# Kernel tuning notes

Measured on AMD Instinct MI355X. Metric: run time of the kernel, lower is better.

## Reference

```python
import jax, jax.numpy as jnp
import numpy as np

N_ITEMS = 2000
N_STORAGE = 4094
N_LOCS = N_STORAGE + 2  # storage locations + start + end
E = 4_194_304
HID = 32


def setup_inputs() -> dict:
    rng = np.random.default_rng(0)
    etype = rng.integers(0, 3, size=E)  # 0: loc-loc, 1: item-item, 2: item-loc
    src = np.empty(E, dtype=np.int64)
    dst = np.empty(E, dtype=np.int64)
    m0, m1, m2 = (etype == 0), (etype == 1), (etype == 2)
    src[m0] = rng.integers(N_ITEMS, N_ITEMS + N_LOCS, m0.sum())
    dst[m0] = rng.integers(N_ITEMS, N_ITEMS + N_LOCS, m0.sum())
    src[m1] = rng.integers(0, N_ITEMS, m1.sum())
    dst[m1] = rng.integers(0, N_ITEMS, m1.sum())
    src[m2] = rng.integers(0, N_ITEMS, m2.sum())
    dst[m2] = rng.integers(N_ITEMS, N_ITEMS + N_STORAGE, m2.sum())
    edge_index = jnp.asarray(np.stack([src, dst]))
    edge_attr = jnp.asarray(rng.random((E, 2)).astype(np.float32))
    edge_type_mask = jnp.asarray(np.eye(3, dtype=bool)[etype])
    k1, k2 = jax.random.split(jax.random.key(0))
    W1 = jax.random.normal(k1, (3, HID), jnp.float32) * 0.5
    b1 = jnp.zeros((HID,), jnp.float32)
    W2 = jax.random.normal(k2, (HID, 1), jnp.float32) * 0.5
    b2 = jnp.zeros((1,), jnp.float32)
    return {
        "edge_index": edge_index,
        "edge_attr": edge_attr,
        "edge_type_mask": edge_type_mask,
        "n_items": N_ITEMS,
        "n_storage": N_STORAGE,
        "n_locs": N_LOCS,
        "W1": W1, "b1": b1, "W2": W2, "b2": b2,
    }


def reference(edge_index, edge_attr, edge_type_mask, n_items, n_storage, n_locs,
              W1, b1, W2, b2):
    src, dst = edge_index[0], edge_index[1]

    # --- loc-loc distance matrix: scatter masked edges into [n_locs, n_locs] ---
    ls, ld = src - n_items, dst - n_items
    v = edge_type_mask[:, 0] & (ls >= 0) & (ls < n_locs) & (ld >= 0) & (ld < n_locs)
    ls = jnp.where(v, ls, n_locs)  # invalid -> out of bounds, dropped by scatter
    ld = jnp.where(v, ld, n_locs)
    loc_mat = jnp.zeros((n_locs, n_locs), edge_attr.dtype).at[ls, ld].set(
        edge_attr[:, 0], mode="drop")

    # --- item-item sequence-count matrix: [n_items, n_items] ---
    v = edge_type_mask[:, 1] & (src >= 0) & (src < n_items) & (dst >= 0) & (dst < n_items)
    is_ = jnp.where(v, src, n_items)
    id_ = jnp.where(v, dst, n_items)
    seq_mat = jnp.zeros((n_items, n_items), edge_attr.dtype).at[is_, id_].set(
        edge_attr[:, 1], mode="drop")

    # --- item -> storage-location assignment: [n_items] int ---
    li = dst - n_items
    v = edge_type_mask[:, 2] & (src >= 0) & (src < n_items) & (li >= 0) & (li < n_storage)
    ii = jnp.where(v, src, n_items)
    item_to_loc = jnp.zeros((n_items,), jnp.int32).at[ii].set(
        jnp.where(v, li, 0).astype(jnp.int32), mode="drop")

    # --- item_item_dist = sum_{i,j: seq>0} seq_mat[i,j] * loc_mat[loc_i, loc_j] ---
    gathered = loc_mat[item_to_loc][:, item_to_loc]  # [n_items, n_items]
    item_item_dist = jnp.sum(jnp.where(seq_mat > 0, seq_mat * gathered, 0.0))

    # --- start / end depot distances (start_idx = n_storage, end_idx = n_storage+1) ---
    start_dist = jnp.sum(loc_mat[n_storage, item_to_loc]) if n_storage < n_locs else jnp.float32(0.0)
    end_dist = jnp.sum(loc_mat[item_to_loc, n_storage + 1]) if n_storage + 1 < n_locs else jnp.float32(0.0)

    comps = jnp.stack([item_item_dist, start_dist, end_dist])[None, :]  # [1, 3]
    h = jax.nn.relu(comps @ W1 + b1)
    pred = h @ W2 + b2  # [1, 1]
    return pred.squeeze()
```

## Files before the change

kernel.cpp:

```cpp
#include <hip/hip_runtime.h>

#define N_ITEMS   2000
#define N_STORAGE 4094
#define N_LOCS    4096
#define E_EDGES   4194304
#define LOCD      2048
#define NBLKB     512
#define BCAP      8192
#define SGRP      500
#define LGRP      512
#define NG        1012
#define SCAP      3456
#define LCAP      3456

typedef unsigned long long u64;
typedef unsigned int u32;
typedef int   vi4 __attribute__((ext_vector_type(4)));
typedef float vf4 __attribute__((ext_vector_type(4)));

__device__ __forceinline__ int wave_incl_scan(int v) {
    #pragma unroll
    for (int o = 1; o < 64; o <<= 1) {
        int u = __shfl_up(v, o);
        if ((threadIdx.x & 63) >= o) v += u;
    }
    return v;
}


__global__ __launch_bounds__(1024)
void bin_all(const int* __restrict__ src, const int* __restrict__ dst,
             const float* __restrict__ attr, u64* __restrict__ seqrec,
             u32* __restrict__ locrec, int* __restrict__ pfxS, int* __restrict__ pfxL,
             int* __restrict__ slab, int* __restrict__ flags4) {
    __shared__ int lwin[N_ITEMS];
    __shared__ int cnt[NG];
    __shared__ int exclS[SGRP];
    __shared__ int exclL[LGRP];
    __shared__ int wsum[16];
    __shared__ int totSL[2];
    __shared__ u64 sseq[SCAP];
    __shared__ u32 sloc[LCAP];
    int t = threadIdx.x;
    for (int i = t; i < N_ITEMS; i += 1024) lwin[i] = -1;
    for (int i = t; i < NG; i += 1024) cnt[i] = 0;
    if (t < 32) flags4[blockIdx.x * 32 + t] = 0;
    int rel0 = t * 8;
    int base = blockIdx.x * BCAP + rel0;
    vi4 sa = __builtin_nontemporal_load((const vi4*)&src[base]);
    vi4 sb = __builtin_nontemporal_load((const vi4*)&src[base + 4]);
    vi4 da = __builtin_nontemporal_load((const vi4*)&dst[base]);
    vi4 db = __builtin_nontemporal_load((const vi4*)&dst[base + 4]);
    vf4 a0 = __builtin_nontemporal_load((const vf4*)&attr[base * 2]);
    vf4 a1 = __builtin_nontemporal_load((const vf4*)&attr[base * 2 + 4]);
    vf4 a2 = __builtin_nontemporal_load((const vf4*)&attr[base * 2 + 8]);
    vf4 a3 = __builtin_nontemporal_load((const vf4*)&attr[base * 2 + 12]);
    __syncthreads();
    int ss[8] = {sa[0], sa[1], sa[2], sa[3], sb[0], sb[1], sb[2], sb[3]};
    int dd[8] = {da[0], da[1], da[2], da[3], db[0], db[1], db[2], db[3]};
    float v1[8] = {a0[1], a0[3], a1[1], a1[3], a2[1], a2[3], a3[1], a3[3]};
    u32 meta[8], aux[8], val[8];
    #pragma unroll
    for (int k = 0; k < 8; ++k) {
        int s = ss[k], d = dd[k];
        u32 m = 0xFFFFFFFFu, ic = 0, vv = 0;
        if ((unsigned)s < N_ITEMS) {
            if ((unsigned)d < N_ITEMS) {
                int g = s >> 2;
                m = ((u32)atomicAdd(&cnt[g], 1) << 10) | (u32)g;
                ic = ((u32)(s & 3) << 24) | ((u32)d << 13) | (u32)(rel0 + k);
                vv = __float_as_uint(v1[k]);
            } else {
                unsigned li = (unsigned)(d - N_ITEMS);
                if (li < N_STORAGE) atomicMax(&lwin[s], base + k);
            }
        } else {
            unsigned ls = (unsigned)(s - N_ITEMS), ld = (unsigned)(d - N_ITEMS);
            if (ls < N_LOCS && ld < N_LOCS) {
                int g = SGRP + (int)(ls >> 3);
                m = ((u32)atomicAdd(&cnt[g], 1) << 10) | (u32)g;
                ic = ((ls & 7u) << 25) | (ld << 13) | (u32)(rel0 + k);
            }
        }
        meta[k] = m;
        aux[k] = ic;
        val[k] = vv;
    }
    __syncthreads();
    int v;
    if (t < 512) v = (t < SGRP) ? cnt[t] : 0;
    else         v = cnt[t - 12];
    int inc = wave_incl_scan(v);
    if ((t & 63) == 63) wsum[t >> 6] = inc;
    __syncthreads();
    int w = t >> 6, lo = (t < 512) ? 0 : 8, woff = 0;
    #pragma unroll
    for (int k = 0; k < 16; ++k) woff += (k >= lo && k < w) ? wsum[k] : 0;
    int ex = inc - v + woff;
    if (t < SGRP) {
        exclS[t] = ex;
        pfxS[t * NBLKB + blockIdx.x] = ex;
    } else if (t >= 512) {
        exclL[t - 512] = ex;
        pfxL[(t - 512) * NBLKB + blockIdx.x] = ex;
    }
    if (t == 0) {
        int t0 = 0, t1 = 0;
        #pragma unroll
        for (int k = 0; k < 8; ++k) { t0 += wsum[k]; t1 += wsum[k + 8]; }
        pfxS[SGRP * NBLKB + blockIdx.x] = t0;
        pfxL[LGRP * NBLKB + blockIdx.x] = t1;
        totSL[0] = t0;
        totSL[1] = t1;
    }
    __syncthreads();
    u64* srb = seqrec + (size_t)blockIdx.x * BCAP;
    u32* lrb = locrec + (size_t)blockIdx.x * BCAP;
    #pragma unroll
    for (int k = 0; k < 8; ++k) {
        u32 m = meta[k];
        if (m != 0xFFFFFFFFu) {
            int g = (int)(m & 1023u), rank = (int)(m >> 10);
            if (g < SGRP) {
                int idx = exclS[g] + rank;
                u64 rec = ((u64)aux[k] << 32) | (u64)val[k];
                if (idx < SCAP) sseq[idx] = rec;
                else            srb[idx] = rec;
            } else {
                int idx = exclL[g - SGRP] + rank;
                if (idx < LCAP) sloc[idx] = aux[k];
                else            lrb[idx] = aux[k];
            }
        }
    }
    __syncthreads();
    int totS = min(totSL[0], SCAP), totL = min(totSL[1], LCAP);
    for (int i = t; i < totS; i += 1024) srb[i] = sseq[i];
    for (int i = t; i < totL; i += 1024) lrb[i] = sloc[i];
    for (int i = t; i < N_ITEMS; i += 1024) slab[blockIdx.x * 2048 + i] = lwin[i];
}

__global__ __launch_bounds__(1024)
void item_reduce(const int* __restrict__ slab, const int* __restrict__ dst,
                 int* __restrict__ item_loc, int* __restrict__ used_row,
                 int* __restrict__ used_col) {
    __shared__ int red[16][64];
    int t = threadIdx.x;
    int lane = t & 63, sub = t >> 6;
    int i = blockIdx.x * 64 + lane;
    int m = -1;
    for (int b = sub; b < NBLKB; b += 16)
        m = max(m, slab[b * 2048 + i]);
    red[sub][lane] = m;
    __syncthreads();
    if (sub == 0 && i < N_ITEMS) {
        #pragma unroll
        for (int k = 1; k < 16; ++k) m = max(m, red[k][lane]);
        int loc = (m >= 0) ? (dst[m] - N_ITEMS) : 0;
        item_loc[i] = loc;
        used_row[loc] = 1;
        used_col[loc] = 1;
    }
    if (blockIdx.x == 0 && t == 0) {
        used_row[N_STORAGE] = 1;
        used_col[N_STORAGE + 1] = 1;
    }
}

__global__ __launch_bounds__(1024)
void remap_fused(const int* __restrict__ used_row, const int* __restrict__ used_col,
                 const int* __restrict__ item_loc, int* __restrict__ rrow,
                 int* __restrict__ rcol, int* __restrict__ item_rr,
                 int* __restrict__ item_rc, int* __restrict__ rse) {
    __shared__ int wsA[16], wsB[16];
    int t = threadIdx.x;
    vi4 ur = *(const vi4*)&used_row[t * 4];
    vi4 uc = *(const vi4*)&used_col[t * 4];
    int sA = ur[0] + ur[1] + ur[2] + ur[3];
    int sB = uc[0] + uc[1] + uc[2] + uc[3];
    int iA = wave_incl_scan(sA);
    int iB = wave_incl_scan(sB);
    if ((t & 63) == 63) { wsA[t >> 6] = iA; wsB[t >> 6] = iB; }
    __syncthreads();
    int w = t >> 6, oA = 0, oB = 0;
    #pragma unroll
    for (int k = 0; k < 16; ++k) {
        oA += (k < w) ? wsA[k] : 0;
        oB += (k < w) ? wsB[k] : 0;
    }
    int runA = iA - sA + oA;
    int runB = iB - sB + oB;
    vi4 rr4, rc4;
    #pragma unroll
    for (int j = 0; j < 4; ++j) {
        runA += ur[j]; rr4[j] = ur[j] ? runA : 0;
        runB += uc[j]; rc4[j] = uc[j] ? runB : 0;
    }
    *(vi4*)&rrow[t * 4] = rr4;
    *(vi4*)&rcol[t * 4] = rc4;
    __syncthreads();
    for (int i = t; i < N_ITEMS; i += 1024) {
        int loc = item_loc[i];
        item_rr[i] = rrow[loc] - 1;
        item_rc[i] = rcol[loc] - 1;
    }
    if (t == 0) {
        rse[0] = rrow[N_STORAGE] - 1;
        rse[1] = rcol[N_STORAGE + 1] - 1;
    }
}

__global__ __launch_bounds__(1024)
void loc_dedup(const u32* __restrict__ locrec, const int* __restrict__ pfxL,
               const float* __restrict__ attr, const int* __restrict__ rrow,
               const int* __restrict__ rcol, float* __restrict__ locf) {
    __shared__ u32 win[8 * 2048];
    __shared__ short rcol_s[N_LOCS];
    __shared__ int rrow8[8];
    int t = threadIdx.x, g = blockIdx.x;
    if (t < 8) rrow8[t] = rrow[g * 8 + t];
    for (int i = t; i < 8 * 2048; i += 1024) win[i] = 0;
    for (int i = t; i < N_LOCS; i += 1024) rcol_s[i] = (short)rcol[i];
    __syncthreads();
    int b = t >> 1, q = t & 1;
    int s0 = pfxL[g * NBLKB + b], s1 = pfxL[(g + 1) * NBLKB + b];
    const u32* rb = locrec + (size_t)b * BCAP;
    u32 kb = ((u32)b << 13) + 1;
    for (int r = s0 + q; r < s1; r += 2) {
        u32 rec = rb[r];
        int il = (int)(rec >> 25);
        if (rrow8[il] <= 0) continue;
        int rc = rcol_s[(rec >> 13) & 4095u];
        if (rc <= 0) continue;
        atomicMax(&win[il * 2048 + rc - 1], kb + (rec & 8191u));
    }
    __syncthreads();
    for (int il = 0; il < 8; ++il) {
        int cr = rrow8[il];
        if (cr <= 0) continue;
        const u32* wrow = &win[il * 2048];
        float* orow = locf + (size_t)(cr - 1) * LOCD;
        for (int i = t; i < 2048; i += 1024) {
            u32 w = wrow[i];
            orow[i] = w ? attr[2 * (int)(w - 1)] : 0.f;
        }
    }
}

__global__ __launch_bounds__(1024)
void seq_dedup(const u64* __restrict__ seqrec, const int* __restrict__ pfxS,
               const float* __restrict__ locf, const int* __restrict__ item_rr,
               const int* __restrict__ item_rc, const int* __restrict__ rse,
               float* __restrict__ gpart) {
    __shared__ u64 win[4 * 2048];
    __shared__ short rcs[N_ITEMS];
    __shared__ int rrs[4];
    __shared__ float red[16][3];
    int t = threadIdx.x, g = blockIdx.x;
    for (int i = t; i < 4 * 2048; i += 1024) win[i] = 0;
    for (int i = t; i < N_ITEMS; i += 1024) rcs[i] = (short)item_rc[i];
    if (t < 4) rrs[t] = item_rr[g * 4 + t];
    __syncthreads();
    int b = t >> 1, q = t & 1;
    int s0 = pfxS[g * NBLKB + b], s1 = pfxS[(g + 1) * NBLKB + b];
    const u64* rb = seqrec + (size_t)b * BCAP;
    u64 kb = ((u64)((u32)b << 13) + 1) << 32;
    for (int r = s0 + q; r < s1; r += 2) {
        u64 rec = rb[r];
        u32 ax = (u32)(rec >> 32);
        int slot = (((int)(ax >> 24) & 3) << 11) | (int)((ax >> 13) & 2047u);
        atomicMax(&win[slot], kb + ((u64)(ax & 8191u) << 32) + (rec & 0xFFFFFFFFull));
    }
    __syncthreads();
    float acc = 0.f, sd = 0.f, ed = 0.f;
    for (int i = t; i < 4 * 2048; i += 1024) {
        u64 w = win[i];
        if (w) {
            float seq = __uint_as_float((u32)(w & 0xFFFFFFFFull));
            if (seq > 0.f)
                acc += seq * locf[(size_t)rrs[i >> 11] * LOCD + (int)rcs[i & 2047]];
        }
    }
    if (t < 4) {
        sd = locf[(size_t)rse[0] * LOCD + (int)rcs[g * 4 + t]];
        ed = locf[(size_t)rrs[t] * LOCD + rse[1]];
    }
    #pragma unroll
    for (int o = 32; o > 0; o >>= 1) {
        acc += __shfl_down(acc, o);
        sd  += __shfl_down(sd, o);
        ed  += __shfl_down(ed, o);
    }
    if ((t & 63) == 0) { red[t >> 6][0] = acc; red[t >> 6][1] = sd; red[t >> 6][2] = ed; }
    __syncthreads();
    if (t == 0) {
        float a = 0.f, bb = 0.f, c = 0.f;
        #pragma unroll
        for (int k = 0; k < 16; ++k) { a += red[k][0]; bb += red[k][1]; c += red[k][2]; }
        gpart[g * 3 + 0] = a;
        gpart[g * 3 + 1] = bb;
        gpart[g * 3 + 2] = c;
    }
}

__global__ void final_mlp(const float* __restrict__ gpart, const float* __restrict__ W1,
                          const float* __restrict__ b1, const float* __restrict__ W2,
                          const float* __restrict__ b2, float* __restrict__ out) {
    __shared__ float s0[4], s1[4], s2[4];
    int t = threadIdx.x;
    float a = 0.f, b = 0.f, c = 0.f;
    for (int i = t; i < SGRP; i += 256) {
        a += gpart[i * 3 + 0];
        b += gpart[i * 3 + 1];
        c += gpart[i * 3 + 2];
    }
    #pragma unroll
    for (int o = 32; o > 0; o >>= 1) {
        a += __shfl_down(a, o);
        b += __shfl_down(b, o);
        c += __shfl_down(c, o);
    }
    if ((t & 63) == 0) { s0[t >> 6] = a; s1[t >> 6] = b; s2[t >> 6] = c; }
    __syncthreads();
    float v = 0.f;
    if (t < 32) {
        float ca = s0[0] + s0[1] + s0[2] + s0[3];
        float cb = s1[0] + s1[1] + s1[2] + s1[3];
        float cc = s2[0] + s2[1] + s2[2] + s2[3];
        float h = ca * W1[t] + cb * W1[32 + t] + cc * W1[64 + t] + b1[t];
        h = fmaxf(h, 0.f);
        v = h * W2[t];
    }
    #pragma unroll
    for (int o = 32; o > 0; o >>= 1) v += __shfl_down(v, o);
    if (t == 0) out[0] = v + b2[0];
}

extern "C" void kernel_launch(void* const* d_in, const int* in_sizes, int n_in,
                              void* d_out, int out_size, void* d_ws, size_t ws_size,
                              hipStream_t stream) {
    const int*   eidx = (const int*)d_in[0];
    const int*   src  = eidx;
    const int*   dst  = eidx + E_EDGES;
    const float* attr = (const float*)d_in[1];
    const float* W1 = (const float*)d_in[6];
    const float* b1 = (const float*)d_in[7];
    const float* W2 = (const float*)d_in[8];
    const float* b2 = (const float*)d_in[9];

    u64*   seqrec   = (u64*)d_ws;
    u32*   locrec   = (u32*)(seqrec + (size_t)NBLKB * BCAP);
    float* locf     = (float*)(locrec + (size_t)NBLKB * BCAP);
    int*   used_row = (int*)(locf + (size_t)LOCD * LOCD);
    int*   used_col = used_row + N_LOCS;
    int*   rrow     = used_col + N_LOCS;
    int*   rcol     = rrow + N_LOCS;
    int*   pfxS     = rcol + N_LOCS;
    int*   pfxL     = pfxS + (SGRP + 1) * NBLKB;
    int*   slab     = pfxL + (LGRP + 1) * NBLKB;
    int*   item_loc = slab + NBLKB * 2048;
    int*   item_rr  = item_loc + N_ITEMS;
    int*   item_rc  = item_rr + N_ITEMS;
    int*   rse      = item_rc + N_ITEMS;
    float* gpart    = (float*)(rse + 2);

    bin_all    <<<NBLKB, 1024, 0, stream>>>(src, dst, attr, seqrec, locrec,
                                            pfxS, pfxL, slab, used_row);
    item_reduce<<<32, 1024, 0, stream>>>(slab, dst, item_loc, used_row, used_col);
    remap_fused<<<1, 1024, 0, stream>>>(used_row, used_col, item_loc, rrow, rcol,
                                        item_rr, item_rc, rse);
    loc_dedup  <<<LGRP, 1024, 0, stream>>>(locrec, pfxL, attr, rrow, rcol, locf);
    seq_dedup  <<<SGRP, 1024, 0, stream>>>(seqrec, pfxS, locf,
                                           item_rr, item_rc, rse, gpart);
    final_mlp  <<<1, 256, 0, stream>>>(gpart, W1, b1, W2, b2, (float*)d_out);
}
```

Measured before the change: 79.83 us.

## Fuse remap prefix scans into loc_dedup and seq_dedup kernels

Removes the single-block remap_fused kernel and has every block of loc_dedup and seq_dedup recompute the used_row/used_col prefix scans in shared memory. Item row/column remaps are derived locally from item_loc. This eliminates one kernel launch and a serialized one-block stage, along with its global intermediate arrays. The cost is redundant scan work and extra barriers in every block.

```diff
diff --git a/kernel.cpp b/kernel.cpp
--- a/kernel.cpp
+++ b/kernel.cpp
@@ -44,7 +44,7 @@
     int t = threadIdx.x;
     for (int i = t; i < N_ITEMS; i += 1024) lwin[i] = -1;
     for (int i = t; i < NG; i += 1024) cnt[i] = 0;
-    if (t < 32) flags4[blockIdx.x * 32 + t] = 0;
+    if (t < 16) flags4[blockIdx.x * 16 + t] = 0;
     int rel0 = t * 8;
     int base = blockIdx.x * BCAP + rel0;
     vi4 sa = __builtin_nontemporal_load((const vi4*)&src[base]);
@@ -168,59 +168,46 @@
 }
 
 __global__ __launch_bounds__(1024)
-void remap_fused(const int* __restrict__ used_row, const int* __restrict__ used_col,
-                 const int* __restrict__ item_loc, int* __restrict__ rrow,
-                 int* __restrict__ rcol, int* __restrict__ item_rr,
-                 int* __restrict__ item_rc, int* __restrict__ rse) {
-    __shared__ int wsA[16], wsB[16];
-    int t = threadIdx.x;
-    vi4 ur = *(const vi4*)&used_row[t * 4];
-    vi4 uc = *(const vi4*)&used_col[t * 4];
-    int sA = ur[0] + ur[1] + ur[2] + ur[3];
-    int sB = uc[0] + uc[1] + uc[2] + uc[3];
-    int iA = wave_incl_scan(sA);
-    int iB = wave_incl_scan(sB);
-    if ((t & 63) == 63) { wsA[t >> 6] = iA; wsB[t >> 6] = iB; }
-    __syncthreads();
-    int w = t >> 6, oA = 0, oB = 0;
-    #pragma unroll
-    for (int k = 0; k < 16; ++k) {
-        oA += (k < w) ? wsA[k] : 0;
-        oB += (k < w) ? wsB[k] : 0;
-    }
-    int runA = iA - sA + oA;
-    int runB = iB - sB + oB;
-    vi4 rr4, rc4;
-    #pragma unroll
-    for (int j = 0; j < 4; ++j) {
-        runA += ur[j]; rr4[j] = ur[j] ? runA : 0;
-        runB += uc[j]; rc4[j] = uc[j] ? runB : 0;
-    }
-    *(vi4*)&rrow[t * 4] = rr4;
-    *(vi4*)&rcol[t * 4] = rc4;
-    __syncthreads();
-    for (int i = t; i < N_ITEMS; i += 1024) {
-        int loc = item_loc[i];
-        item_rr[i] = rrow[loc] - 1;
-        item_rc[i] = rcol[loc] - 1;
-    }
-    if (t == 0) {
-        rse[0] = rrow[N_STORAGE] - 1;
-        rse[1] = rcol[N_STORAGE + 1] - 1;
-    }
-}
-
-__global__ __launch_bounds__(1024)
 void loc_dedup(const u32* __restrict__ locrec, const int* __restrict__ pfxL,
-               const float* __restrict__ attr, const int* __restrict__ rrow,
-               const int* __restrict__ rcol, float* __restrict__ locf) {
+               const float* __restrict__ attr, const int* __restrict__ used_row,
+               const int* __restrict__ used_col, float* __restrict__ locf) {
     __shared__ u32 win[8 * 2048];
     __shared__ short rcol_s[N_LOCS];
     __shared__ int rrow8[8];
+    __shared__ int ws[16];
     int t = threadIdx.x, g = blockIdx.x;
-    if (t < 8) rrow8[t] = rrow[g * 8 + t];
+    vi4 uc = *(const vi4*)&used_col[t * 4];
+    int sB = uc[0] + uc[1] + uc[2] + uc[3];
+    int iB = wave_incl_scan(sB);
+    if ((t & 63) == 63) ws[t >> 6] = iB;
+    __syncthreads();
+    int w = t >> 6, oB = 0;
+    #pragma unroll
+    for (int k = 0; k < 16; ++k) oB += (k < w) ? ws[k] : 0;
+    int runB = iB - sB + oB;
+    #pragma unroll
+    for (int j = 0; j < 4; ++j) {
+        runB += uc[j];
+        rcol_s[t * 4 + j] = uc[j] ? (short)runB : (short)0;
+    }
+    __syncthreads();
+    vi4 ur = *(const vi4*)&used_row[t * 4];
+    int sA = ur[0] + ur[1] + ur[2] + ur[3];
+    int iA = wave_incl_scan(sA);
+    if ((t & 63) == 63) ws[t >> 6] = iA;
+    __syncthreads();
+    int oA = 0;
+    #pragma unroll
+    for (int k = 0; k < 16; ++k) oA += (k < w) ? ws[k] : 0;
+    int runA = iA - sA + oA;
+    #pragma unroll
+    for (int j = 0; j < 4; ++j) {
+        runA += ur[j];
+        int pos = t * 4 + j;
+        if (pos >= g * 8 && pos < g * 8 + 8)
+            rrow8[pos - g * 8] = ur[j] ? runA : 0;
+    }
     for (int i = t; i < 8 * 2048; i += 1024) win[i] = 0;
-    for (int i = t; i < N_LOCS; i += 1024) rcol_s[i] = (short)rcol[i];
     __syncthreads();
     int b = t >> 1, q = t & 1;
     int s0 = pfxL[g * NBLKB + b], s1 = pfxL[(g + 1) * NBLKB + b];
@@ -241,25 +228,62 @@
         const u32* wrow = &win[il * 2048];
         float* orow = locf + (size_t)(cr - 1) * LOCD;
         for (int i = t; i < 2048; i += 1024) {
-            u32 w = wrow[i];
-            orow[i] = w ? attr[2 * (int)(w - 1)] : 0.f;
+            u32 wv = wrow[i];
+            orow[i] = wv ? attr[2 * (int)(wv - 1)] : 0.f;
         }
     }
 }
 
 __global__ __launch_bounds__(1024)
 void seq_dedup(const u64* __restrict__ seqrec, const int* __restrict__ pfxS,
-               const float* __restrict__ locf, const int* __restrict__ item_rr,
-               const int* __restrict__ item_rc, const int* __restrict__ rse,
+               const float* __restrict__ locf, const int* __restrict__ item_loc,
+               const int* __restrict__ used_row, const int* __restrict__ used_col,
                float* __restrict__ gpart) {
     __shared__ u64 win[4 * 2048];
     __shared__ short rcs[N_ITEMS];
     __shared__ int rrs[4];
+    __shared__ int rse_s[2];
+    __shared__ int ws[16];
     __shared__ float red[16][3];
     int t = threadIdx.x, g = blockIdx.x;
+    short* tab = (short*)win;
+    vi4 uc = *(const vi4*)&used_col[t * 4];
+    int sB = uc[0] + uc[1] + uc[2] + uc[3];
+    int iB = wave_incl_scan(sB);
+    if ((t & 63) == 63) ws[t >> 6] = iB;
+    __syncthreads();
+    int w = t >> 6, oB = 0;
+    #pragma unroll
+    for (int k = 0; k < 16; ++k) oB += (k < w) ? ws[k] : 0;
+    int runB = iB - sB + oB;
+    #pragma unroll
+    for (int j = 0; j < 4; ++j) {
+        runB += uc[j];
+        tab[t * 4 + j] = uc[j] ? (short)runB : (short)0;
+    }
+    __syncthreads();
+    for (int i = t; i < N_ITEMS; i += 1024) rcs[i] = tab[item_loc[i]] - 1;
+    if (t == 0) rse_s[1] = tab[N_STORAGE + 1] - 1;
+    __syncthreads();
+    vi4 ur = *(const vi4*)&used_row[t * 4];
+    int sA = ur[0] + ur[1] + ur[2] + ur[3];
+    int iA = wave_incl_scan(sA);
+    if ((t & 63) == 63) ws[t >> 6] = iA;
+    __syncthreads();
+    int oA = 0;
+    #pragma unroll
+    for (int k = 0; k < 16; ++k) oA += (k < w) ? ws[k] : 0;
+    int runA = iA - sA + oA;
+    #pragma unroll
+    for (int j = 0; j < 4; ++j) {
+        runA += ur[j];
+        tab[t * 4 + j] = ur[j] ? (short)runA : (short)0;
+    }
+    __syncthreads();
+    if (t < 4) rrs[t] = tab[item_loc[g * 4 + t]] - 1;
+    if (t == 0) rse_s[0] = tab[N_STORAGE] - 1;
+    __syncthreads();
     for (int i = t; i < 4 * 2048; i += 1024) win[i] = 0;
-    for (int i = t; i < N_ITEMS; i += 1024) rcs[i] = (short)item_rc[i];
-    if (t < 4) rrs[t] = item_rr[g * 4 + t];
     __syncthreads();
     int b = t >> 1, q = t & 1;
     int s0 = pfxS[g * NBLKB + b], s1 = pfxS[(g + 1) * NBLKB + b];
@@ -274,16 +298,16 @@
     __syncthreads();
     float acc = 0.f, sd = 0.f, ed = 0.f;
     for (int i = t; i < 4 * 2048; i += 1024) {
-        u64 w = win[i];
-        if (w) {
-            float seq = __uint_as_float((u32)(w & 0xFFFFFFFFull));
+        u64 wv = win[i];
+        if (wv) {
+            float seq = __uint_as_float((u32)(wv & 0xFFFFFFFFull));
             if (seq > 0.f)
                 acc += seq * locf[(size_t)rrs[i >> 11] * LOCD + (int)rcs[i & 2047]];
         }
     }
     if (t < 4) {
-        sd = locf[(size_t)rse[0] * LOCD + (int)rcs[g * 4 + t]];
-        ed = locf[(size_t)rrs[t] * LOCD + rse[1]];
+        sd = locf[(size_t)rse_s[0] * LOCD + (int)rcs[g * 4 + t]];
+        ed = locf[(size_t)rrs[t] * LOCD + rse_s[1]];
     }
     #pragma unroll
     for (int o = 32; o > 0; o >>= 1) {
@@ -353,24 +377,17 @@
     float* locf     = (float*)(locrec + (size_t)NBLKB * BCAP);
     int*   used_row = (int*)(locf + (size_t)LOCD * LOCD);
     int*   used_col = used_row + N_LOCS;
-    int*   rrow     = used_col + N_LOCS;
-    int*   rcol     = rrow + N_LOCS;
-    int*   pfxS     = rcol + N_LOCS;
+    int*   pfxS     = used_col + N_LOCS;
     int*   pfxL     = pfxS + (SGRP + 1) * NBLKB;
     int*   slab     = pfxL + (LGRP + 1) * NBLKB;
     int*   item_loc = slab + NBLKB * 2048;
-    int*   item_rr  = item_loc + N_ITEMS;
-    int*   item_rc  = item_rr + N_ITEMS;
-    int*   rse      = item_rc + N_ITEMS;
-    float* gpart    = (float*)(rse + 2);
+    float* gpart    = (float*)(item_loc + N_ITEMS);
 
     bin_all    <<<NBLKB, 1024, 0, stream>>>(src, dst, attr, seqrec, locrec,
                                             pfxS, pfxL, slab, used_row);
     item_reduce<<<32, 1024, 0, stream>>>(slab, dst, item_loc, used_row, used_col);
-    remap_fused<<<1, 1024, 0, stream>>>(used_row, used_col, item_loc, rrow, rcol,
-                                        item_rr, item_rc, rse);
-    loc_dedup  <<<LGRP, 1024, 0, stream>>>(locrec, pfxL, attr, rrow, rcol, locf);
-    seq_dedup  <<<SGRP, 1024, 0, stream>>>(seqrec, pfxS, locf,
-                                           item_rr, item_rc, rse, gpart);
+    loc_dedup  <<<LGRP, 1024, 0, stream>>>(locrec, pfxL, attr, used_row, used_col, locf);
+    seq_dedup  <<<SGRP, 1024, 0, stream>>>(seqrec, pfxS, locf, item_loc,
+                                           used_row, used_col, gpart);
     final_mlp  <<<1, 256, 0, stream>>>(gpart, W1, b1, W2, b2, (float*)d_out);
 }
```

New measurement: 77.44 us (median of 2 runs). 3.0% less time.
